# Optimization experiments

Hardware: AMD Instinct MI355X
Metric: run time of the kernel (lower is better)

## Reference

```python
import jax, jax.numpy as jnp
import numpy as np


def setup_inputs() -> dict:
    key = jax.random.key(0)
    k_x, k_wxh, k_whh, k_fcw, k_fcb = jax.random.split(key, 5)
    B, T, I, H = 256, 512, 64, 512
    x = jax.random.normal(k_x, (B, T, I), dtype=jnp.float32)
    W_xh = jax.random.normal(k_wxh, (I, H), dtype=jnp.float32) * 0.01
    W_hh = jax.random.normal(k_whh, (H, H), dtype=jnp.float32) * 0.01
    b = jnp.zeros((H,), dtype=jnp.float32)
    # nn.Linear(H, 1): weight (1, H), bias (1); init ~ U(-1/sqrt(H), 1/sqrt(H))
    lim = 1.0 / np.sqrt(H)
    fc_w = jax.random.uniform(k_fcw, (1, H), dtype=jnp.float32, minval=-lim, maxval=lim)
    fc_b = jax.random.uniform(k_fcb, (1,), dtype=jnp.float32, minval=-lim, maxval=lim)
    return {"x": x, "W_xh": W_xh, "W_hh": W_hh, "b": b, "fc_w": fc_w, "fc_b": fc_b}


def reference(x, W_xh, W_hh, b, fc_w, fc_b):
    B, T, I = x.shape
    H = W_hh.shape[0]
    # Precompute input projections for all timesteps in one big matmul: (B,T,H)
    xh = jnp.einsum('bti,ih->bth', x, W_xh) + b
    h0 = jnp.zeros((B, H), dtype=x.dtype)

    def step(h, xh_t):
        h_new = jnp.tanh(xh_t + h @ W_hh)
        return h_new, None

    h_final, _ = jax.lax.scan(step, h0, jnp.swapaxes(xh, 0, 1))  # scan over T
    return h_final @ fc_w.T + fc_b  # (B, 1)
```

## Files before the change

### kernel.cpp

```cpp
#include <hip/hip_runtime.h>

#define BATCH    256
#define TSTEPS   512
#define IDIM     64
#define HDIM     512
#define KEXT     576
#define NTHREADS 512
#define REG_PAIRS  224
#define REG_CHUNKS 56
#define LDS_CHUNKS 16
#define LDSW_STRIDE 17

#define LDSW_BYTES (512 * LDSW_STRIDE * 16)
#define HBUF_OFF   LDSW_BYTES
#define HBUF_ELEMS 640
#define RED_OFF    (HBUF_OFF + 2 * HBUF_ELEMS * 2)
#define SMEM_BYTES (RED_OFF + 64)

typedef _Float16 half2_t __attribute__((ext_vector_type(2)));
typedef _Float16 half8_t __attribute__((ext_vector_type(8)));

union H8U {
    half8_t v;
    half2_t p[4];
    uint4   u4;
};

__device__ __forceinline__ float fdot2(half2_t a, half2_t b, float c) {
#if __has_builtin(__builtin_amdgcn_fdot2)
    return __builtin_amdgcn_fdot2(a, b, c, false);
#else
    return c + (float)a[0] * (float)b[0] + (float)a[1] * (float)b[1];
#endif
}

__device__ __forceinline__ float fast_tanh(float x) {
    float e = __builtin_amdgcn_exp2f(x * 2.88539008177792681472f);
    return 1.0f - 2.0f * __builtin_amdgcn_rcpf(e + 1.0f);
}

__global__ __launch_bounds__(NTHREADS, 2)
void rnn_persist(const float* __restrict__ x,
                 const float* __restrict__ Wxh,
                 const float* __restrict__ Whh,
                 const float* __restrict__ bias,
                 const float* __restrict__ fcw,
                 const float* __restrict__ fcb,
                 float* __restrict__ out)
{
    extern __shared__ char smem[];
    uint4*     ldsW = reinterpret_cast<uint4*>(smem);
    _Float16*  hbuf = reinterpret_cast<_Float16*>(smem + HBUF_OFF);
    float*     red  = reinterpret_cast<float*>(smem + RED_OFF);

    const int j = threadIdx.x;
    const int b = blockIdx.x;

    half2_t wreg[REG_PAIRS];
#pragma unroll
    for (int p = 0; p < REG_PAIRS; ++p) {
        const int k = 2 * p;
        half2_t w;
        w[0] = (_Float16)Whh[(size_t)k * HDIM + j];
        w[1] = (_Float16)Whh[(size_t)(k + 1) * HDIM + j];
        wreg[p] = w;
    }
#pragma unroll
    for (int cc = 0; cc < LDS_CHUNKS; ++cc) {
        H8U u;
#pragma unroll
        for (int q = 0; q < 4; ++q) {
            const int k0 = 448 + 8 * cc + 2 * q;
            const int k1 = k0 + 1;
            half2_t w;
            w[0] = (_Float16)(k0 < HDIM ? Whh[(size_t)k0 * HDIM + j]
                                        : Wxh[(size_t)(k0 - HDIM) * HDIM + j]);
            w[1] = (_Float16)(k1 < HDIM ? Whh[(size_t)k1 * HDIM + j]
                                        : Wxh[(size_t)(k1 - HDIM) * HDIM + j]);
            u.p[q] = w;
        }
        ldsW[j * LDSW_STRIDE + cc] = u.u4;
    }

    const float bj   = bias[j];
    const float fcwj = fcw[j];

    hbuf[j] = (_Float16)0.0f;
    if (j < IDIM) hbuf[HDIM + j] = (_Float16)x[((size_t)b * TSTEPS + 0) * IDIM + j];
    __syncthreads();

    float hval = 0.0f;
    for (int t = 0; t < TSTEPS; ++t) {
        const int cur = t & 1;
        const int nxt = cur ^ 1;
        const _Float16* hb = hbuf + cur * HBUF_ELEMS;

        float xv = 0.0f;
        const bool do_x = (j < IDIM) && (t + 1 < TSTEPS);
        if (do_x) xv = x[((size_t)b * TSTEPS + (t + 1)) * IDIM + j];

        float a0 = bj, a1 = 0.0f, a2 = 0.0f, a3 = 0.0f;
#pragma unroll
        for (int c = 0; c < REG_CHUNKS; ++c) {
            H8U u;
            u.v = *reinterpret_cast<const half8_t*>(hb + 8 * c);
            a0 = fdot2(u.p[0], wreg[4 * c + 0], a0);
            a1 = fdot2(u.p[1], wreg[4 * c + 1], a1);
            a2 = fdot2(u.p[2], wreg[4 * c + 2], a2);
            a3 = fdot2(u.p[3], wreg[4 * c + 3], a3);
        }
#pragma unroll
        for (int cc = 0; cc < LDS_CHUNKS; ++cc) {
            H8U u, w;
            u.v  = *reinterpret_cast<const half8_t*>(hb + 8 * (REG_CHUNKS + cc));
            w.u4 = ldsW[j * LDSW_STRIDE + cc];
            a0 = fdot2(u.p[0], w.p[0], a0);
            a1 = fdot2(u.p[1], w.p[1], a1);
            a2 = fdot2(u.p[2], w.p[2], a2);
            a3 = fdot2(u.p[3], w.p[3], a3);
        }
        const float a = (a0 + a1) + (a2 + a3);
        hval = fast_tanh(a);

        hbuf[nxt * HBUF_ELEMS + j] = (_Float16)hval;
        if (do_x) hbuf[nxt * HBUF_ELEMS + HDIM + j] = (_Float16)xv;
        __syncthreads();
    }

    float partial = hval * fcwj;
#pragma unroll
    for (int off = 32; off >= 1; off >>= 1)
        partial += __shfl_down(partial, off, 64);
    if ((j & 63) == 0) red[j >> 6] = partial;
    __syncthreads();
    if (j == 0) {
        float s = 0.0f;
#pragma unroll
        for (int w = 0; w < 8; ++w) s += red[w];
        out[b] = s + fcb[0];
    }
}

extern "C" void kernel_launch(void* const* d_in, const int* in_sizes, int n_in,
                              void* d_out, int out_size, void* d_ws, size_t ws_size,
                              hipStream_t stream) {
    const float* x    = (const float*)d_in[0];
    const float* Wxh  = (const float*)d_in[1];
    const float* Whh  = (const float*)d_in[2];
    const float* bias = (const float*)d_in[3];
    const float* fcw  = (const float*)d_in[4];
    const float* fcb  = (const float*)d_in[5];
    float* out = (float*)d_out;

    hipFuncSetAttribute(reinterpret_cast<const void*>(rnn_persist),
                        hipFuncAttributeMaxDynamicSharedMemorySize, SMEM_BYTES);

    rnn_persist<<<BATCH, NTHREADS, SMEM_BYTES, stream>>>(x, Wxh, Whh, bias, fcw, fcb, out);
}
```

Before: 1.298 ms.

## Split input projection into a separate GEMM kernel feeding the recurrent loop

Adds an xh_gemm kernel that precomputes x@W_xh+b for all timesteps into a half-precision workspace buffer. The recurrent kernel then only does the 512-wide h@W_hh dot product and adds the precomputed value, so the inner loop shrinks from K=576 to K=512. The register/LDS split of W_hh is retuned for both paths, and a fused fallback with different split sizes is kept for when the workspace is too small. In exchange it writes and reads a 128 MB fp16 intermediate through global memory and launches one more kernel.

```diff
diff --git a/kernel.cpp b/kernel.cpp
--- a/kernel.cpp
+++ b/kernel.cpp
@@ -1,21 +1,11 @@
 #include <hip/hip_runtime.h>
+
 
 #define BATCH    256
 #define TSTEPS   512
 #define IDIM     64
 #define HDIM     512
-#define KEXT     576
-#define NTHREADS 512
-#define REG_PAIRS  224
-#define REG_CHUNKS 56
-#define LDS_CHUNKS 16
-#define LDSW_STRIDE 17
-
-#define LDSW_BYTES (512 * LDSW_STRIDE * 16)
-#define HBUF_OFF   LDSW_BYTES
-#define HBUF_ELEMS 640
-#define RED_OFF    (HBUF_OFF + 2 * HBUF_ELEMS * 2)
-#define SMEM_BYTES (RED_OFF + 64)
+#define NTH      512
 
 typedef _Float16 half2_t __attribute__((ext_vector_type(2)));
 typedef _Float16 half8_t __attribute__((ext_vector_type(8)));
@@ -39,26 +29,55 @@
     return 1.0f - 2.0f * __builtin_amdgcn_rcpf(e + 1.0f);
 }
 
-__global__ __launch_bounds__(NTHREADS, 2)
-void rnn_persist(const float* __restrict__ x,
-                 const float* __restrict__ Wxh,
-                 const float* __restrict__ Whh,
-                 const float* __restrict__ bias,
-                 const float* __restrict__ fcw,
-                 const float* __restrict__ fcb,
-                 float* __restrict__ out)
+#define XH_ROWS 16
+__global__ __launch_bounds__(NTH, 4)
+void xh_gemm(const float* __restrict__ x, const float* __restrict__ Wxh,
+             const float* __restrict__ bias, _Float16* __restrict__ xh)
+{
+    const int j = threadIdx.x;
+    const size_t r0 = (size_t)blockIdx.x * XH_ROWS;
+    float wcol[IDIM];
+#pragma unroll
+    for (int i = 0; i < IDIM; ++i) wcol[i] = Wxh[(size_t)i * HDIM + j];
+    const float bj = bias[j];
+#pragma unroll
+    for (int r = 0; r < XH_ROWS; ++r) {
+        const float* xr = x + (r0 + r) * IDIM;
+        float acc = bj;
+#pragma unroll
+        for (int i = 0; i < IDIM; ++i) acc += xr[i] * wcol[i];
+        xh[(r0 + r) * HDIM + j] = (_Float16)acc;
+    }
+}
+
+#define S_RP   208
+#define S_RC   52
+#define S_LC   12
+#define S_LSTR 13
+#define S_LDSW_BYTES (512 * S_LSTR * 16)
+#define S_HBUF_OFF   S_LDSW_BYTES
+#define S_HBUF_ELEMS 512
+#define S_RED_OFF    (S_HBUF_OFF + 2 * S_HBUF_ELEMS * 2)
+#define S_SMEM_BYTES (S_RED_OFF + 64)
+
+__global__ __attribute__((amdgpu_flat_work_group_size(NTH, NTH), amdgpu_waves_per_eu(2, 2)))
+void rnn_split(const _Float16* __restrict__ xh,
+               const float* __restrict__ Whh,
+               const float* __restrict__ fcw,
+               const float* __restrict__ fcb,
+               float* __restrict__ out)
 {
     extern __shared__ char smem[];
-    uint4*     ldsW = reinterpret_cast<uint4*>(smem);
-    _Float16*  hbuf = reinterpret_cast<_Float16*>(smem + HBUF_OFF);
-    float*     red  = reinterpret_cast<float*>(smem + RED_OFF);
+    uint4*    ldsW = reinterpret_cast<uint4*>(smem);
+    _Float16* hbuf = reinterpret_cast<_Float16*>(smem + S_HBUF_OFF);
+    float*    red  = reinterpret_cast<float*>(smem + S_RED_OFF);
 
     const int j = threadIdx.x;
     const int b = blockIdx.x;
 
-    half2_t wreg[REG_PAIRS];
-#pragma unroll
-    for (int p = 0; p < REG_PAIRS; ++p) {
+    half2_t wreg[S_RP];
+#pragma unroll
+    for (int p = 0; p < S_RP; ++p) {
         const int k = 2 * p;
         half2_t w;
         w[0] = (_Float16)Whh[(size_t)k * HDIM + j];
@@ -66,11 +85,112 @@
         wreg[p] = w;
     }
 #pragma unroll
-    for (int cc = 0; cc < LDS_CHUNKS; ++cc) {
+    for (int cc = 0; cc < S_LC; ++cc) {
         H8U u;
 #pragma unroll
         for (int q = 0; q < 4; ++q) {
-            const int k0 = 448 + 8 * cc + 2 * q;
+            const int k0 = 416 + 8 * cc + 2 * q;
+            half2_t w;
+            w[0] = (_Float16)Whh[(size_t)k0 * HDIM + j];
+            w[1] = (_Float16)Whh[(size_t)(k0 + 1) * HDIM + j];
+            u.p[q] = w;
+        }
+        ldsW[j * S_LSTR + cc] = u.u4;
+    }
+
+    const float fcwj = fcw[j];
+    const _Float16* xhb = xh + (size_t)b * TSTEPS * HDIM;
+
+    hbuf[j] = (_Float16)0.0f;
+    __syncthreads();
+
+    float hval = 0.0f;
+    for (int t = 0; t < TSTEPS; ++t) {
+        const int cur = t & 1;
+        const int nxt = cur ^ 1;
+        const _Float16* hb = hbuf + cur * S_HBUF_ELEMS;
+
+        const float xv = (float)xhb[(size_t)t * HDIM + j];
+
+        float a0 = 0.0f, a1 = 0.0f, a2 = 0.0f, a3 = 0.0f;
+#pragma unroll
+        for (int c = 0; c < S_RC; ++c) {
+            H8U u;
+            u.v = *reinterpret_cast<const half8_t*>(hb + 8 * c);
+            a0 = fdot2(u.p[0], wreg[4 * c + 0], a0);
+            a1 = fdot2(u.p[1], wreg[4 * c + 1], a1);
+            a2 = fdot2(u.p[2], wreg[4 * c + 2], a2);
+            a3 = fdot2(u.p[3], wreg[4 * c + 3], a3);
+        }
+#pragma unroll
+        for (int cc = 0; cc < S_LC; ++cc) {
+            H8U u, w;
+            u.v  = *reinterpret_cast<const half8_t*>(hb + 8 * (S_RC + cc));
+            w.u4 = ldsW[j * S_LSTR + cc];
+            a0 = fdot2(u.p[0], w.p[0], a0);
+            a1 = fdot2(u.p[1], w.p[1], a1);
+            a2 = fdot2(u.p[2], w.p[2], a2);
+            a3 = fdot2(u.p[3], w.p[3], a3);
+        }
+        hval = fast_tanh(((a0 + a1) + (a2 + a3)) + xv);
+
+        hbuf[nxt * S_HBUF_ELEMS + j] = (_Float16)hval;
+        __syncthreads();
+    }
+
+    float partial = hval * fcwj;
+#pragma unroll
+    for (int off = 32; off >= 1; off >>= 1)
+        partial += __shfl_down(partial, off, 64);
+    if ((j & 63) == 0) red[j >> 6] = partial;
+    __syncthreads();
+    if (j == 0) {
+        float s = 0.0f;
+#pragma unroll
+        for (int w = 0; w < 8; ++w) s += red[w];
+        out[b] = s + fcb[0];
+    }
+}
+
+#define F_RP   216
+#define F_RC   54
+#define F_LC   18
+#define F_LSTR 19
+#define F_LDSW_BYTES (512 * F_LSTR * 16)
+#define F_HBUF_OFF   F_LDSW_BYTES
+#define F_HBUF_ELEMS 640
+#define F_RED_OFF    (F_HBUF_OFF + 2 * F_HBUF_ELEMS * 2)
+#define F_SMEM_BYTES (F_RED_OFF + 64)
+
+__global__ __attribute__((amdgpu_flat_work_group_size(NTH, NTH), amdgpu_waves_per_eu(2, 2)))
+void rnn_fused(const float* __restrict__ x, const float* __restrict__ Wxh,
+               const float* __restrict__ Whh, const float* __restrict__ bias,
+               const float* __restrict__ fcw, const float* __restrict__ fcb,
+               float* __restrict__ out)
+{
+    extern __shared__ char smem[];
+    uint4*    ldsW = reinterpret_cast<uint4*>(smem);
+    _Float16* hbuf = reinterpret_cast<_Float16*>(smem + F_HBUF_OFF);
+    float*    red  = reinterpret_cast<float*>(smem + F_RED_OFF);
+
+    const int j = threadIdx.x;
+    const int b = blockIdx.x;
+
+    half2_t wreg[F_RP];
+#pragma unroll
+    for (int p = 0; p < F_RP; ++p) {
+        const int k = 2 * p;
+        half2_t w;
+        w[0] = (_Float16)Whh[(size_t)k * HDIM + j];
+        w[1] = (_Float16)Whh[(size_t)(k + 1) * HDIM + j];
+        wreg[p] = w;
+    }
+#pragma unroll
+    for (int cc = 0; cc < F_LC; ++cc) {
+        H8U u;
+#pragma unroll
+        for (int q = 0; q < 4; ++q) {
+            const int k0 = 432 + 8 * cc + 2 * q;
             const int k1 = k0 + 1;
             half2_t w;
             w[0] = (_Float16)(k0 < HDIM ? Whh[(size_t)k0 * HDIM + j]
@@ -79,7 +199,7 @@
                                         : Wxh[(size_t)(k1 - HDIM) * HDIM + j]);
             u.p[q] = w;
         }
-        ldsW[j * LDSW_STRIDE + cc] = u.u4;
+        ldsW[j * F_LSTR + cc] = u.u4;
     }
 
     const float bj   = bias[j];
@@ -93,7 +213,7 @@
     for (int t = 0; t < TSTEPS; ++t) {
         const int cur = t & 1;
         const int nxt = cur ^ 1;
-        const _Float16* hb = hbuf + cur * HBUF_ELEMS;
+        const _Float16* hb = hbuf + cur * F_HBUF_ELEMS;
 
         float xv = 0.0f;
         const bool do_x = (j < IDIM) && (t + 1 < TSTEPS);
@@ -101,7 +221,7 @@
 
         float a0 = bj, a1 = 0.0f, a2 = 0.0f, a3 = 0.0f;
 #pragma unroll
-        for (int c = 0; c < REG_CHUNKS; ++c) {
+        for (int c = 0; c < F_RC; ++c) {
             H8U u;
             u.v = *reinterpret_cast<const half8_t*>(hb + 8 * c);
             a0 = fdot2(u.p[0], wreg[4 * c + 0], a0);
@@ -110,20 +230,19 @@
             a3 = fdot2(u.p[3], wreg[4 * c + 3], a3);
         }
 #pragma unroll
-        for (int cc = 0; cc < LDS_CHUNKS; ++cc) {
+        for (int cc = 0; cc < F_LC; ++cc) {
             H8U u, w;
-            u.v  = *reinterpret_cast<const half8_t*>(hb + 8 * (REG_CHUNKS + cc));
-            w.u4 = ldsW[j * LDSW_STRIDE + cc];
+            u.v  = *reinterpret_cast<const half8_t*>(hb + 8 * (F_RC + cc));
+            w.u4 = ldsW[j * F_LSTR + cc];
             a0 = fdot2(u.p[0], w.p[0], a0);
             a1 = fdot2(u.p[1], w.p[1], a1);
             a2 = fdot2(u.p[2], w.p[2], a2);
             a3 = fdot2(u.p[3], w.p[3], a3);
         }
-        const float a = (a0 + a1) + (a2 + a3);
-        hval = fast_tanh(a);
-
-        hbuf[nxt * HBUF_ELEMS + j] = (_Float16)hval;
-        if (do_x) hbuf[nxt * HBUF_ELEMS + HDIM + j] = (_Float16)xv;
+        hval = fast_tanh((a0 + a1) + (a2 + a3));
+
+        hbuf[nxt * F_HBUF_ELEMS + j] = (_Float16)hval;
+        if (do_x) hbuf[nxt * F_HBUF_ELEMS + HDIM + j] = (_Float16)xv;
         __syncthreads();
     }
 
@@ -152,8 +271,16 @@
     const float* fcb  = (const float*)d_in[5];
     float* out = (float*)d_out;
 
-    hipFuncSetAttribute(reinterpret_cast<const void*>(rnn_persist),
-                        hipFuncAttributeMaxDynamicSharedMemorySize, SMEM_BYTES);
-
-    rnn_persist<<<BATCH, NTHREADS, SMEM_BYTES, stream>>>(x, Wxh, Whh, bias, fcw, fcb, out);
-}
+    const size_t xh_bytes = (size_t)BATCH * TSTEPS * HDIM * sizeof(_Float16);
+    if (ws_size >= xh_bytes) {
+        hipFuncSetAttribute(reinterpret_cast<const void*>(rnn_split),
+                            hipFuncAttributeMaxDynamicSharedMemorySize, S_SMEM_BYTES);
+        _Float16* xh = (_Float16*)d_ws;
+        xh_gemm<<<(BATCH * TSTEPS) / XH_ROWS, NTH, 0, stream>>>(x, Wxh, bias, xh);
+        rnn_split<<<BATCH, NTH, S_SMEM_BYTES, stream>>>(xh, Whh, fcw, fcb, out);
+    } else {
+        hipFuncSetAttribute(reinterpret_cast<const void*>(rnn_fused),
+                            hipFuncAttributeMaxDynamicSharedMemorySize, F_SMEM_BYTES);
+        rnn_fused<<<BATCH, NTH, F_SMEM_BYTES, stream>>>(x, Wxh, Whh, bias, fcw, fcb, out);
+    }
+}
```

Result: faster. 1.152 ms (-11.2%).
